# Optimization experiments

Measured on AMD Instinct MI355X. Metric: run time of the kernel, lower is better.

The kernel has to match this reference:

```python
import jax, jax.numpy as jnp
import numpy as np


def spatial_coords(h, w):
    # Vectorized generate_spatial_batch -> [8, h, w]
    ws = jnp.arange(w, dtype=jnp.float32)
    hs = jnp.arange(h, dtype=jnp.float32)
    xmin = ws / w * 2 - 1
    xmax = (ws + 1) / w * 2 - 1
    ymin = hs / h * 2 - 1
    ymax = (hs + 1) / h * 2 - 1
    z = jnp.zeros((h, w), jnp.float32)
    return jnp.stack([
        z + xmin[None, :], z + ymin[:, None], z + xmax[None, :], z + ymax[:, None],
        z + (xmin + xmax)[None, :] / 2, z + (ymin + ymax)[:, None] / 2,
        z + 1.0 / w, z + 1.0 / h], axis=0)


def conv3x3(x, w):
    return jax.lax.conv_general_dilated(x, w, (1, 1), [(1, 1), (1, 1)],
                                        dimension_numbers=('NCHW', 'OIHW', 'NCHW'))


def conv1x1(x, w, b=None):
    y = jnp.einsum('nchw,dc->ndhw', x, w)
    return y if b is None else y + b[None, :, None, None]


def _forward(f_nodes, h_nodes, p_nodes, xp, h_att, p_att,
             dc_q_w, dc_q_b, dc_k_w, dc_k_b, dc_p_w, dc_p_b,
             ctx_w1, ctx_w2, ctx_b2,
             du_a1, du_a2, du_a2b, du_r1, du_r2,
             dl_a1, dl_a2, dl_a2b, dl_r1, dl_r2,
             dp_proj, dp_r1, dp_r2, dp_r2b,
             gru_gw, gru_gb, gru_cw, alpha):
    # BatchNorm (InPlaceABNSync) at default init is identity; relu(leaky_relu(x)) == relu(x).
    N, C, H, W = xp.shape
    coord = spatial_coords(H, W)                      # [8,H,W]
    coord_b = jnp.broadcast_to(coord[None], (N, 8, H, W))
    # Dep_Context: shared key map
    key_f = jax.nn.relu(conv1x1(jnp.concatenate([xp, coord_b], axis=1), dc_k_w, dc_k_b))  # [N,64,H,W]
    xp_flat = xp.reshape(N, C, H * W)
    coord_flat = coord.reshape(8, H * W)
    wq, wk = dc_p_w[:, :64], dc_p_w[:, 64:]           # split project conv over concat channels

    def dep_context(hu_att):                          # hu_att: [N,1,H,W]
        na = jax.nn.softmax(hu_att.reshape(N, H * W), axis=-1)
        hu_c = jnp.einsum('nck,nk->nc', xp_flat, na)  # attention-pooled center [N,C]
        co_c = jnp.einsum('ck,nk->nc', coord_flat, na)
        q = jax.nn.relu(jnp.concatenate([hu_c, co_c], axis=1) @ dc_q_w.T + dc_q_b)  # [N,64]
        energy = (q @ wq.T)[:, :, None, None] + conv1x1(key_f, wk) + dc_p_b[None, :, None, None]
        att = jax.nn.sigmoid(energy)                  # [N,1,H,W]
        inv = 1.0 - hu_att
        return att * inv, att * xp * inv

    dep_att, dep = jax.vmap(dep_context)(p_att[1:])   # [6,N,1,H,W], [6,N,C,H,W]

    # Contexture attention maps (per-part weights); 5 = neighbors per node in full graph
    def ctx_att(da, w1, w2, b2):
        h1 = jax.nn.relu(conv3x3(jnp.concatenate([da, xp], axis=1), w1))
        return conv1x1(h1, w2, b2)                    # [N,5,H,W]

    fdep_att = jax.vmap(ctx_att)(dep_att, ctx_w1, ctx_w2, ctx_b2)  # [6,N,5,H,W]
    att_sm = jax.nn.softmax(fdep_att, axis=2)

    def decomp(parent, children, parent_att, a1, a2, a2b, r1, r2):
        dm = conv1x1(jax.nn.relu(conv3x3(jnp.concatenate([parent_att, xp], axis=1), a1)), a2, a2b)
        da = jax.nn.softmax(dm, axis=1)               # [N,K,H,W]
        def rel(att_i, child):
            x = jnp.concatenate([parent * att_i * parent_att, child], axis=1)
            return jax.nn.relu(conv1x1(jax.nn.relu(conv3x3(x, r1)), r2))
        parts = jax.vmap(rel)(jnp.moveaxis(da, 1, 0)[:, :, None], children)
        return parts, dm

    du_parts, du_att = decomp(h_nodes[1], p_nodes[1:5], h_att[1], du_a1, du_a2, du_a2b, du_r1, du_r2)
    dl_parts, dl_att = decomp(h_nodes[2], p_nodes[5:7], h_att[2], dl_a1, dl_a2, dl_a2b, dl_r1, dl_r2)

    # Dependency messages over the fixed part graph (fully connected, 6 part nodes)
    P = 6
    ea, eb = np.nonzero(1 - np.eye(P, dtype=np.int32))   # row-major == torch.nonzero order
    ce = np.where(eb < ea, eb, eb - 1)                   # index of b in part_list_list[a]
    hv_e = p_nodes[eb]        # NOTE: source indexes p_node_list by raw edge id (no +1) - kept faithful
    hu_e = dep[ea]            # [E,N,C,H,W]
    att_e = att_sm[ea, :, ce][:, :, None]                # [E,N,1,H,W]

    def dep_msg(hv, hu, att):
        m = jax.nn.relu(conv1x1(hu * att, dp_proj))
        y = jax.nn.relu(conv3x3(jnp.concatenate([m, hv], axis=1), dp_r1))
        return jax.nn.sigmoid(conv1x1(y, dp_r2, dp_r2b))

    msgs = jax.vmap(dep_msg)(hv_e, hu_e, att_e)          # [E,N,hid,H,W]
    xpp = jax.ops.segment_sum(msgs, jnp.asarray(eb), num_segments=P)  # [6,N,hid,H,W]

    x_stack = jnp.concatenate([h_nodes[0:1],
                               du_parts + alpha * xpp[0:4],
                               dl_parts + alpha * xpp[4:6]], axis=0)   # [7,N,hid,H,W]

    def gru(x, h, gw, gb, cw):
        g = conv1x1(jnp.concatenate([x, h], axis=1), gw, gb)
        r = jax.nn.sigmoid(g[:, 0:1])
        u = jax.nn.sigmoid(g[:, 1:2])
        cnm = jax.nn.relu(conv1x1(jnp.concatenate([x, r * h], axis=1), cw))
        return (1 - u) * h + u * cnm

    p_new = jax.vmap(gru)(x_stack, p_nodes, gru_gw, gru_gb, gru_cw)
    return (p_new, du_att, dl_att, fdep_att)


def setup_inputs() -> dict:
    key = jax.random.key(0)
    ks = iter(jax.random.split(key, 48))
    def rn(shape, s=0.05):
        return jax.random.normal(next(ks), shape, jnp.float32) * s
    N, C, H, W, HID, P = 2, 256, 48, 48, 10, 7
    return dict(
        f_nodes=rn((2, N, HID, H, W), 1.0),
        h_nodes=rn((3, N, HID, H, W), 1.0),
        p_nodes=rn((P, N, HID, H, W), 1.0),
        xp=rn((N, C, H, W), 1.0),
        h_att=jax.random.uniform(next(ks), (3, N, 1, H, W), jnp.float32),
        p_att=jax.random.uniform(next(ks), (P, N, 1, H, W), jnp.float32),
        dc_q_w=rn((64, C + 8)), dc_q_b=jnp.zeros((64,), jnp.float32),
        dc_k_w=rn((64, C + 8)), dc_k_b=jnp.zeros((64,), jnp.float32),
        dc_p_w=rn((1, 128)), dc_p_b=jnp.zeros((1,), jnp.float32),
        ctx_w1=rn((6, C, C + 1, 3, 3)), ctx_w2=rn((6, 5, C)), ctx_b2=jnp.zeros((6, 5), jnp.float32),
        du_a1=rn((C, C + 1, 3, 3)), du_a2=rn((4, C)), du_a2b=jnp.zeros((4,), jnp.float32),
        du_r1=rn((HID, 2 * HID, 3, 3)), du_r2=rn((HID, HID)),
        dl_a1=rn((C, C + 1, 3, 3)), dl_a2=rn((2, C)), dl_a2b=jnp.zeros((2,), jnp.float32),
        dl_r1=rn((HID, 2 * HID, 3, 3)), dl_r2=rn((HID, HID)),
        dp_proj=rn((HID, C)), dp_r1=rn((HID, 2 * HID, 3, 3)), dp_r2=rn((HID, HID)), dp_r2b=jnp.zeros((HID,), jnp.float32),
        gru_gw=rn((P, 2, 2 * HID)), gru_gb=jnp.zeros((P, 2), jnp.float32), gru_cw=rn((P, HID, 2 * HID)),
        alpha=jnp.ones((1,), jnp.float32),
    )


def reference(f_nodes, h_nodes, p_nodes, xp, h_att, p_att,
              dc_q_w, dc_q_b, dc_k_w, dc_k_b, dc_p_w, dc_p_b,
              ctx_w1, ctx_w2, ctx_b2,
              du_a1, du_a2, du_a2b, du_r1, du_r2,
              dl_a1, dl_a2, dl_a2b, dl_r1, dl_r2,
              dp_proj, dp_r1, dp_r2, dp_r2b,
              gru_gw, gru_gb, gru_cw, alpha):
    return _forward(f_nodes, h_nodes, p_nodes, xp, h_att, p_att,
                    dc_q_w, dc_q_b, dc_k_w, dc_k_b, dc_p_w, dc_p_b,
                    ctx_w1, ctx_w2, ctx_b2,
                    du_a1, du_a2, du_a2b, du_r1, du_r2,
                    dl_a1, dl_a2, dl_a2b, dl_r1, dl_r2,
                    dp_proj, dp_r1, dp_r2, dp_r2b,
                    gru_gw, gru_gb, gru_cw, alpha)
```

## Files before the change

kernel.cpp:

```cpp
#include <hip/hip_runtime.h>
#include <math.h>

constexpr int NB_ = 2;
constexpr int C_  = 256;
constexpr int HW_ = 2304;

typedef float f32x4 __attribute__((ext_vector_type(4)));
typedef short short8 __attribute__((ext_vector_type(8)));

__device__ __forceinline__ float coordval(int c, int k) {
  int y = k / 48, x = k - y * 48;
  switch (c) {
    case 0: return x * (1.f/24.f) - 1.f;
    case 1: return y * (1.f/24.f) - 1.f;
    case 2: return (x + 1) * (1.f/24.f) - 1.f;
    case 3: return (y + 1) * (1.f/24.f) - 1.f;
    case 4: return (x + 0.5f) * (1.f/24.f) - 1.f;
    case 5: return (y + 0.5f) * (1.f/24.f) - 1.f;
    default: return 1.f/48.f;
  }
}

__device__ __forceinline__ float sigmoidf_(float x) { return 1.f / (1.f + expf(-x)); }
__device__ __forceinline__ unsigned short f2bf(float f) {
  unsigned int u = __float_as_uint(f);
  unsigned int r = (u + 0x7FFFu + ((u >> 16) & 1u)) >> 16;
  return (unsigned short)r;
}
__device__ __forceinline__ float bf2f(unsigned short h) {
  return __uint_as_float(((unsigned int)h) << 16);
}

__device__ __forceinline__ void xbf_impl(int bid, char* smem,
    const float* __restrict__ xp, unsigned short* __restrict__ xbf)
{
  float (*xt)[65] = (float(*)[65])smem;
  int t = threadIdx.x;
  int px0 = bid * 64;
  int n = px0 / HW_, k0 = px0 - n * HW_;
  for (int cb = 0; cb < 4; ++cb) {
    __syncthreads();
    for (int i = t; i < 4096; i += 256) {
      int cl = i >> 6, pxl = i & 63;
      xt[cl][pxl] = xp[((size_t)(n * C_ + cb * 64 + cl)) * HW_ + k0 + pxl];
    }
    __syncthreads();
    for (int i = t; i < 4096; i += 256) {
      int pxl = i >> 6, cl = i & 63;
      xbf[((size_t)(n * HW_ + k0 + pxl)) * 256 + cb * 64 + cl] = f2bf(xt[cl][pxl]);
    }
  }
}

__device__ __forceinline__ void wbf_impl(int bid, char* smem,
    const float* __restrict__ ctx_w1, const float* __restrict__ du_a1,
    const float* __restrict__ dl_a1,
    unsigned short* __restrict__ wt, float* __restrict__ w0)
{
  float* sl = (float*)smem;
  int inst = bid >> 8, oc = bid & 255;
  const float* src = (inst < 6) ? (ctx_w1 + (size_t)inst * 256 * 2313)
                   : (inst == 6 ? du_a1 : dl_a1);
  src += (size_t)oc * 2313;
  int t = threadIdx.x;
  for (int i = t; i < 2313; i += 256) sl[i] = src[i];
  __syncthreads();
  int mf = oc >> 4, lr = oc & 15;
  for (int i = t; i < 288; i += 256) {
    int pos = i / 32; int rest = i - pos * 32;
    int chunk = rest >> 2, lg = rest & 3;
    short8 v;
    #pragma unroll
    for (int j = 0; j < 8; ++j) {
      int c = chunk * 32 + lg * 8 + j;
      v[j] = (short)f2bf(sl[(size_t)(c + 1) * 9 + pos]);
    }
    size_t addr = ((((size_t)(inst * 9 + pos) * 8 + chunk) * 16 + mf) << 9)
                  + (size_t)(lg * 16 + lr) * 8;
    *(short8*)(wt + addr) = v;
  }
  if (t < 9) w0[((size_t)inst * 256 + oc) * 9 + t] = sl[t];
}

__device__ __forceinline__ void smhuc_impl(int bid, char* smem,
    const float* __restrict__ xp, const float* __restrict__ p_att,
    float* __restrict__ hu_ws)
{
  float* na  = (float*)smem;
  float* red = (float*)(smem + 9216);
  int cb = bid & 15; int pair = bid >> 4;
  int n = pair % NB_;
  int t = threadIdx.x;
  const float* att = p_att + (size_t)(NB_ + pair) * HW_;

  float m = -1e30f;
  for (int k = t; k < HW_; k += 256) m = fmaxf(m, att[k]);
  #pragma unroll
  for (int off = 32; off > 0; off >>= 1) m = fmaxf(m, __shfl_down(m, off, 64));
  if ((t & 63) == 0) red[t >> 6] = m;
  __syncthreads();
  if (t == 0) { float mm = red[0]; for (int w = 1; w < 4; ++w) mm = fmaxf(mm, red[w]); red[0] = mm; }
  __syncthreads();
  m = red[0];
  float s = 0.f;
  for (int k = t; k < HW_; k += 256) s += expf(att[k] - m);
  #pragma unroll
  for (int off = 32; off > 0; off >>= 1) s += __shfl_down(s, off, 64);
  if ((t & 63) == 0) red[8 + (t >> 6)] = s;
  __syncthreads();
  if (t == 0) { float ss = 0; for (int w = 0; w < 4; ++w) ss += red[8 + w]; red[8] = ss; }
  __syncthreads();
  float inv = 1.f / red[8];
  for (int k = t; k < HW_; k += 256) na[k] = expf(att[k] - m) * inv;
  __syncthreads();

  int wv = t >> 6, l = t & 63;
  #pragma unroll
  for (int cq = 0; cq < 4; ++cq) {
    int c = cb * 16 + wv * 4 + cq;
    const float* x = xp + (size_t)(n * C_ + c) * HW_;
    float a = 0.f;
    for (int k = l; k < HW_; k += 64) a = fmaf(x[k], na[k], a);
    #pragma unroll
    for (int off = 32; off > 0; off >>= 1) a += __shfl_down(a, off, 64);
    if (l == 0) hu_ws[(size_t)pair * 256 + c] = a;
  }
}

__device__ __forceinline__ void yhv_impl(int bid, char* smem,
    const float* __restrict__ p_nodes, const float* __restrict__ dp_r1,
    float* __restrict__ yhv_ws)
{
  float (*xt)[18][20] = (float(*)[18][20])smem;
  float* wl = (float*)(smem + 14400);
  int tile = bid % 9; bid /= 9;
  int n = bid % NB_;  int v = bid / NB_;
  int ty0 = (tile / 3) * 16, tx0 = (tile % 3) * 16;
  int t = threadIdx.x;
  for (int i = t; i < 900; i += 256) {
    int d = i / 90; int rest = i - d * 90; int ic = rest / 9; int pos = rest - ic * 9;
    wl[i] = dp_r1[(d * 20 + 10 + ic) * 9 + pos];
  }
  for (int i = t; i < 10 * 324; i += 256) {
    int d = i / 324; int rr = (i % 324) / 18; int cc = i % 18;
    int gy = ty0 + rr - 1, gx = tx0 + cc - 1;
    float val = 0.f;
    if (gy >= 0 && gy < 48 && gx >= 0 && gx < 48)
      val = p_nodes[((size_t)(v * NB_ + n) * 10 + d) * HW_ + gy * 48 + gx];
    xt[d][rr][cc] = val;
  }
  __syncthreads();
  int rr = t >> 4, cc = t & 15;
  int k = (ty0 + rr) * 48 + tx0 + cc;
  float y[10];
  #pragma unroll
  for (int d = 0; d < 10; ++d) y[d] = 0.f;
  for (int ic = 0; ic < 10; ++ic)
    #pragma unroll
    for (int kh = 0; kh < 3; ++kh)
      #pragma unroll
      for (int kw = 0; kw < 3; ++kw) {
        float xv = xt[ic][rr + kh][cc + kw];
        #pragma unroll
        for (int d = 0; d < 10; ++d)
          y[d] = fmaf(wl[(d * 10 + ic) * 9 + kh * 3 + kw], xv, y[d]);
      }
  #pragma unroll
  for (int d = 0; d < 10; ++d)
    yhv_ws[((size_t)(v * NB_ + n) * 10 + d) * HW_ + k] = y[d];
}

__global__ __launch_bounds__(256) void k_fa(
    const float* __restrict__ xp, unsigned short* __restrict__ xbf,
    const float* __restrict__ ctx_w1, const float* __restrict__ du_a1,
    const float* __restrict__ dl_a1,
    unsigned short* __restrict__ wt, float* __restrict__ w0,
    const float* __restrict__ p_att, float* __restrict__ hu_ws,
    const float* __restrict__ p_nodes, const float* __restrict__ dp_r1,
    float* __restrict__ yhv_ws)
{
  __shared__ __align__(16) char smem[18432];
  int bid = blockIdx.x;
  if (bid < 72)        xbf_impl(bid, smem, xp, xbf);
  else if (bid < 2120) wbf_impl(bid - 72, smem, ctx_w1, du_a1, dl_a1, wt, w0);
  else if (bid < 2312) smhuc_impl(bid - 2120, smem, xp, p_att, hu_ws);
  else                 yhv_impl(bid - 2312, smem, p_nodes, dp_r1, yhv_ws);
}

__device__ __forceinline__ void qdot_impl(int pair, char* smem,
    const float* __restrict__ p_att, const float* __restrict__ hu_ws,
    const float* __restrict__ dc_q_w, const float* __restrict__ dc_q_b,
    const float* __restrict__ dc_p_w, float* __restrict__ qdot)
{
  float* na  = (float*)smem;
  float* red = (float*)(smem + 9216);
  float* co  = (float*)(smem + 9280);
  float* hu  = (float*)(smem + 9312);
  float* ql  = (float*)(smem + 10336);
  int t = threadIdx.x;
  const float* att = p_att + (size_t)(NB_ + pair) * HW_;

  float m = -1e30f;
  for (int k = t; k < HW_; k += 256) m = fmaxf(m, att[k]);
  #pragma unroll
  for (int off = 32; off > 0; off >>= 1) m = fmaxf(m, __shfl_down(m, off, 64));
  if ((t & 63) == 0) red[t >> 6] = m;
  __syncthreads();
  if (t == 0) { float mm = red[0]; for (int w = 1; w < 4; ++w) mm = fmaxf(mm, red[w]); red[0] = mm; }
  __syncthreads();
  m = red[0];
  float s = 0.f;
  for (int k = t; k < HW_; k += 256) s += expf(att[k] - m);
  #pragma unroll
  for (int off = 32; off > 0; off >>= 1) s += __shfl_down(s, off, 64);
  if ((t & 63) == 0) red[8 + (t >> 6)] = s;
  __syncthreads();
  if (t == 0) { float ss = 0; for (int w = 0; w < 4; ++w) ss += red[8 + w]; red[8] = ss; }
  __syncthreads();
  float inv = 1.f / red[8];
  for (int k = t; k < HW_; k += 256) na[k] = expf(att[k] - m) * inv;
  hu[t] = hu_ws[(size_t)pair * 256 + t];
  __syncthreads();

  int wv = t >> 6, l = t & 63;
  #pragma unroll
  for (int q = 0; q < 2; ++q) {
    int cc = wv * 2 + q;
    float a = 0.f;
    for (int k = l; k < HW_; k += 64) a = fmaf(coordval(cc, k), na[k], a);
    #pragma unroll
    for (int off = 32; off > 0; off >>= 1) a += __shfl_down(a, off, 64);
    if (l == 0) co[cc] = a;
  }
  __syncthreads();
  if (t < 64) {
    float a = dc_q_b[t];
    const float* wr = dc_q_w + (size_t)t * 264;
    for (int c = 0; c < 256; ++c) a = fmaf(wr[c], hu[c], a);
    #pragma unroll
    for (int c = 0; c < 8; ++c) a = fmaf(wr[256 + c], co[c], a);
    ql[t] = fmaxf(a, 0.f) * dc_p_w[t];
  }
  __syncthreads();
  if (t == 0) {
    float a = 0.f;
    for (int d = 0; d < 64; ++d) a += ql[d];
    qdot[pair] = a;
  }
}

__device__ __forceinline__ void rpx_impl(int bid, char* smem,
    const unsigned short* __restrict__ xbf, const float* __restrict__ dp_proj,
    float* __restrict__ rpx)
{
  float* pj   = (float*)smem;
  float* part = (float*)(smem + 10240);
  int t = threadIdx.x;
  for (int i = t; i < 2560; i += 256) {
    int d = i >> 8, c = i & 255;
    pj[c * 10 + d] = dp_proj[i];
  }
  __syncthreads();
  int lane = t & 63, q = t >> 6;
  int px = bid * 64 + lane;
  const unsigned short* xr = xbf + (size_t)px * 256;
  float acc[10];
  #pragma unroll
  for (int d = 0; d < 10; ++d) acc[d] = 0.f;
  for (int c8 = q * 8; c8 < q * 8 + 8; ++c8) {
    short8 v = *(const short8*)(xr + c8 * 8);
    #pragma unroll
    for (int j = 0; j < 8; ++j) {
      float f = bf2f((unsigned short)v[j]);
      const float* pc = &pj[(c8 * 8 + j) * 10];
      #pragma unroll
      for (int d = 0; d < 10; ++d) acc[d] = fmaf(pc[d], f, acc[d]);
    }
  }
  if (q) {
    #pragma unroll
    for (int d = 0; d < 10; ++d) part[((q - 1) * 64 + lane) * 10 + d] = acc[d];
  }
  __syncthreads();
  if (t < 64) {
    int p2 = bid * 64 + t;
    int n = p2 / HW_, k = p2 - n * HW_;
    #pragma unroll
    for (int d = 0; d < 10; ++d) {
      float s = acc[d] + part[t * 10 + d] + part[(64 + t) * 10 + d] + part[(128 + t) * 10 + d];
      rpx[((size_t)(n * 10 + d)) * HW_ + k] = fmaxf(s, 0.f);
    }
  }
}

__global__ __launch_bounds__(256) void k_fb(
    const float* __restrict__ p_att, const float* __restrict__ hu_ws,
    const float* __restrict__ dc_q_w, const float* __restrict__ dc_q_b,
    const float* __restrict__ dc_p_w, float* __restrict__ qdot,
    const unsigned short* __restrict__ xbf, const float* __restrict__ dp_proj,
    float* __restrict__ rpx)
{
  __shared__ __align__(16) char smem[18432];
  int bid = blockIdx.x;
  if (bid < 12) qdot_impl(bid, smem, p_att, hu_ws, dc_q_w, dc_q_b, dc_p_w, qdot);
  else          rpx_impl(bid - 12, smem, xbf, dp_proj, rpx);
}

__global__ __launch_bounds__(256) void k_keymma(
    const unsigned short* __restrict__ xbf, const float* __restrict__ dc_k_w,
    const float* __restrict__ dc_k_b, const float* __restrict__ dc_p_w,
    const float* __restrict__ qdot, const float* __restrict__ dc_p_b,
    const float* __restrict__ p_att, float* __restrict__ dep_att)
{
  __shared__ unsigned short wlf[64 * 296];
  __shared__ unsigned short xl[64 * 40];
  int t = threadIdx.x;
  for (int i = t; i < 64 * 264; i += 256) {
    int d = i / 264, c = i - d * 264;
    wlf[d * 296 + c] = f2bf(dc_k_w[i]);
  }
  for (int i = t; i < 64 * 32; i += 256) {
    int d = i >> 5, c = 264 + (i & 31);
    wlf[d * 296 + c] = 0;
  }
  int px0 = blockIdx.x * 64;
  int w = t >> 6, l = t & 63;
  int lr = l & 15, lg = l >> 4;

  f32x4 acc[4];
  #pragma unroll
  for (int mi = 0; mi < 4; ++mi) acc[mi] = (f32x4){0.f,0.f,0.f,0.f};

  for (int ch = 0; ch < 9; ++ch) {
    __syncthreads();
    {
      int i = t;
      int pxl = i >> 2, q = i & 3;
      int px = px0 + pxl, n = px / HW_, k = px - n * HW_;
      int c0 = ch * 32 + q * 8;
      short8 v;
      if (c0 + 7 < 256) {
        v = *(const short8*)(xbf + ((size_t)(n * HW_ + k)) * 256 + c0);
      } else {
        #pragma unroll
        for (int j = 0; j < 8; ++j) {
          int cc = c0 + j;
          float f = (cc < 256) ? bf2f(xbf[((size_t)(n * HW_ + k)) * 256 + cc])
                   : (cc < 264 ? coordval(cc - 256, k) : 0.f);
          v[j] = (short)f2bf(f);
        }
      }
      *(short8*)(xl + pxl * 40 + q * 8) = v;
    }
    __syncthreads();
    short8 bfr = *(const short8*)(xl + (w * 16 + lr) * 40 + lg * 8);
    #pragma unroll
    for (int mi = 0; mi < 4; ++mi) {
      short8 a = *(const short8*)(wlf + (mi * 16 + lr) * 296 + ch * 32 + lg * 8);
      acc[mi] = __builtin_amdgcn_mfma_f32_16x16x32_bf16(a, bfr, acc[mi], 0, 0, 0);
    }
  }

  float s = 0.f;
  #pragma unroll
  for (int mi = 0; mi < 4; ++mi)
    #pragma unroll
    for (int r = 0; r < 4; ++r) {
      int d = mi * 16 + lg * 4 + r;
      s += dc_p_w[64 + d] * fmaxf(acc[mi][r] + dc_k_b[d], 0.f);
    }
  s += __shfl_down(s, 32, 64);
  s += __shfl_down(s, 16, 64);
  if (lg == 0) {
    int px = px0 + w * 16 + lr;
    int n = px / HW_, k = px - n * HW_;
    float base = s + dc_p_b[0];
    #pragma unroll
    for (int e = 0; e < 6; ++e) {
      float energy = qdot[e * NB_ + n] + base;
      float a = sigmoidf_(energy);
      float hu = p_att[(size_t)((1 + e) * NB_ + n) * HW_ + k];
      dep_att[((size_t)(e * NB_ + n)) * HW_ + k] = a * (1.f - hu);
    }
  }
}

__global__ __launch_bounds__(512, 4) void k_convfused(
    const unsigned short* __restrict__ xbf, const unsigned short* __restrict__ wt,
    const float* __restrict__ w0, const float* __restrict__ dep_att,
    const float* __restrict__ h_att,
    const float* __restrict__ ctx_w2, const float* __restrict__ du_a2,
    const float* __restrict__ dl_a2,
    const float* __restrict__ ctx_b2, const float* __restrict__ du_a2b,
    const float* __restrict__ dl_a2b,
    float* __restrict__ out_fdep, float* __restrict__ out_du, float* __restrict__ out_dl,
    float* __restrict__ att_sm, float* __restrict__ da_u, float* __restrict__ da_l)
{
  int bid = blockIdx.x;
  int inst = bid & 7;
  int n = (bid >> 3) & 1;
  int tile = bid >> 4;
  int ty0 = (tile >> 3) * 8;
  int tx0 = (tile & 7) * 6;

  __shared__ __align__(16) unsigned short xs[80 * 256];
  __shared__ float asf[80];

  const float* asrc = (inst < 6) ? dep_att + (size_t)(inst * NB_ + n) * HW_
                    : h_att + (size_t)(((inst == 6) ? 1 : 2) * NB_ + n) * HW_;
  int nd = (inst < 6) ? 5 : (inst == 6 ? 4 : 2);
  const float* w2 = (inst < 6) ? ctx_w2 + (size_t)inst * 5 * 256
                               : (inst == 6 ? du_a2 : dl_a2);

  int t = threadIdx.x;
  const unsigned short* xg = xbf + (size_t)n * HW_ * 256;

  for (int i = t; i < 2560; i += 512) {
    int row = i >> 5, q = i & 31;
    int yy = row >> 3, xx = row & 7;
    int gy = ty0 + yy - 1, gx = tx0 + xx - 1;
    short8 v = (short8){0,0,0,0,0,0,0,0};
    if (gy >= 0 && gy < 48 && gx >= 0 && gx < 48)
      v = *(const short8*)(xg + ((size_t)(gy * 48 + gx)) * 256 + q * 8);
    int s = q ^ (row & 7);
    *(short8*)(xs + row * 256 + s * 8) = v;
  }
  for (int i = t; i < 80; i += 512) {
    int yy = i >> 3, xx = i & 7;
    int gy = ty0 + yy - 1, gx = tx0 + xx - 1;
    asf[i] = (gy >= 0 && gy < 48 && gx >= 0 && gx < 48) ? asrc[gy * 48 + gx] : 0.f;
  }
  __syncthreads();

  int wm = t >> 6;
  int l = t & 63;
  int lr = l & 15, lg = l >> 4;

  f32x4 acc[2][3];
  #pragma unroll
  for (int mi = 0; mi < 2; ++mi)
    #pragma unroll
    for (int nf = 0; nf < 3; ++nf) acc[mi][nf] = (f32x4){0.f,0.f,0.f,0.f};

  int rb[3];
  #pragma unroll
  for (int nf = 0; nf < 3; ++nf) {
    int p = nf * 16 + lr;
    int y = p / 6, x = p - y * 6;
    rb[nf] = y * 8 + x;
  }

  const unsigned short* wta = wt + (((size_t)inst * 72 * 16) << 9)
                              + (((size_t)(wm * 2)) << 9) + (size_t)l * 8;
  short8 av[2], nv[2];
  av[0] = *(const short8*)(wta);
  av[1] = *(const short8*)(wta + 512);

  for (int ch = 0; ch < 8; ++ch) {
    #pragma unroll
    for (int pos = 0; pos < 9; ++pos) {
      {
        int npos = (pos == 8) ? 0 : pos + 1;
        int nch = (pos == 8) ? ((ch + 1 > 7) ? 7 : ch + 1) : ch;
        size_t ofs = ((size_t)((npos * 8 + nch) * 16)) << 9;
        nv[0] = *(const short8*)(wta + ofs);
        nv[1] = *(const short8*)(wta + ofs + 512);
      }
      int koff = (pos / 3) * 8 + (pos % 3);
      short8 bfr[3];
      #pragma unroll
      for (int nf = 0; nf < 3; ++nf) {
        int rowIdx = rb[nf] + koff;
        int s = (ch * 4 + lg) ^ (rowIdx & 7);
        bfr[nf] = *(const short8*)(xs + rowIdx * 256 + s * 8);
      }
      #pragma unroll
      for (int mi = 0; mi < 2; ++mi)
        #pragma unroll
        for (int nf = 0; nf < 3; ++nf)
          acc[mi][nf] = __builtin_amdgcn_mfma_f32_16x16x32_bf16(av[mi], bfr[nf], acc[mi][nf], 0, 0, 0);
      av[0] = nv[0]; av[1] = nv[1];
    }
  }

  __syncthreads();
  float* ovl = (float*)xs;
  float* w0l = ovl;
  float* w2l = ovl + 2304;
  float* sred = ovl + 3584;
  for (int i = t; i < 2304; i += 512) w0l[i] = w0[(size_t)inst * 2304 + i];
  for (int i = t; i < 1280; i += 512) w2l[i] = (i < nd * 256) ? w2[i] : 0.f;
  __syncthreads();

  float pd[3][5];
  #pragma unroll
  for (int nf = 0; nf < 3; ++nf)
    #pragma unroll
    for (int d = 0; d < 5; ++d) pd[nf][d] = 0.f;

  #pragma unroll
  for (int nf = 0; nf < 3; ++nf) {
    #pragma unroll
    for (int mi = 0; mi < 2; ++mi) {
      #pragma unroll
      for (int r = 0; r < 4; ++r) {
        int oc = wm * 32 + mi * 16 + lg * 4 + r;
        float v = acc[mi][nf][r];
        const float* wr = &w0l[oc * 9];
        #pragma unroll
        for (int pos = 0; pos < 9; ++pos) {
          int koff = (pos / 3) * 8 + (pos % 3);
          v = fmaf(wr[pos], asf[rb[nf] + koff], v);
        }
        v = fmaxf(v, 0.f);
        #pragma unroll
        for (int d = 0; d < 5; ++d) pd[nf][d] = fmaf(w2l[d * 256 + oc], v, pd[nf][d]);
      }
    }
  }
  #pragma unroll
  for (int nf = 0; nf < 3; ++nf)
    #pragma unroll
    for (int d = 0; d < 5; ++d) {
      float s = pd[nf][d];
      s += __shfl_down(s, 32, 64);
      s += __shfl_down(s, 16, 64);
      pd[nf][d] = s;
    }
  if (lg == 0) {
    #pragma unroll
    for (int nf = 0; nf < 3; ++nf) {
      int pxi = nf * 16 + lr;
      #pragma unroll
      for (int d = 0; d < 5; ++d)
        sred[(wm * 48 + pxi) * 5 + d] = pd[nf][d];
    }
  }
  __syncthreads();
  if (t < 48) {
    int y = t / 6, x = t - y * 6;
    int gk = (ty0 + y) * 48 + tx0 + x;
    float vals[5];
    float mx = -1e30f;
    for (int d = 0; d < nd; ++d) {
      float s = 0.f;
      #pragma unroll
      for (int wq = 0; wq < 8; ++wq) s += sred[(wq * 48 + t) * 5 + d];
      s += (inst < 6) ? ctx_b2[inst * 5 + d] : (inst == 6 ? du_a2b[d] : dl_a2b[d]);
      vals[d] = s;
      mx = fmaxf(mx, s);
      if (inst < 6)       out_fdep[((size_t)(inst * NB_ + n) * 5 + d) * HW_ + gk] = s;
      else if (inst == 6) out_du[((size_t)n * 4 + d) * HW_ + gk] = s;
      else                out_dl[((size_t)n * 2 + d) * HW_ + gk] = s;
    }
    float ssum = 0.f;
    for (int d = 0; d < nd; ++d) { vals[d] = expf(vals[d] - mx); ssum += vals[d]; }
    float is = 1.f / ssum;
    for (int d = 0; d < nd; ++d) {
      float sm = vals[d] * is;
      if (inst < 6)       att_sm[((size_t)(inst * NB_ + n) * 5 + d) * HW_ + gk] = sm;
      else if (inst == 6) da_u[((size_t)n * 4 + d) * HW_ + gk] = sm;
      else                da_l[((size_t)n * 2 + d) * HW_ + gk] = sm;
    }
  }
}

__global__ __launch_bounds__(256) void k_msgs_edge(
    const float* __restrict__ att_sm, const float* __restrict__ dep_att,
    const float* __restrict__ rpx, const float* __restrict__ yhv_ws,
    const float* __restrict__ dp_r1, const float* __restrict__ dp_r2,
    const float* __restrict__ dp_r2b, float* __restrict__ msg_ws)
{
  int b = blockIdx.x;
  int tile = b % 9; b /= 9;
  int n = b % NB_;  b /= NB_;
  int ui = b % 5;   int v = b / 5;
  int u = (ui < v) ? ui : ui + 1;
  int ce = (v < u) ? v : v - 1;
  int ty0 = (tile / 3) * 16, tx0 = (tile % 3) * 16;

  __shared__ float xt[10][18][20];
  __shared__ float wl[900];
  __shared__ float w2l[100];
  __shared__ float b2l[10];
  int t = threadIdx.x;
  for (int i = t; i < 900; i += 256) {
    int d = i / 90; int rest = i - d * 90; int ic = rest / 9; int pos = rest - ic * 9;
    wl[i] = dp_r1[(d * 20 + ic) * 9 + pos];
  }
  for (int i = t; i < 100; i += 256) w2l[i] = dp_r2[i];
  if (t < 10) b2l[t] = dp_r2b[t];

  const float* asrc = att_sm + ((size_t)(u * NB_ + n) * 5 + ce) * HW_;
  const float* dsrc = dep_att + (size_t)(u * NB_ + n) * HW_;
  for (int i = t; i < 10 * 324; i += 256) {
    int d = i / 324; int rr = (i % 324) / 18; int cc = i % 18;
    int gy = ty0 + rr - 1, gx = tx0 + cc - 1;
    float val = 0.f;
    if (gy >= 0 && gy < 48 && gx >= 0 && gx < 48) {
      int kk = gy * 48 + gx;
      val = asrc[kk] * dsrc[kk] * rpx[((size_t)n * 10 + d) * HW_ + kk];
    }
    xt[d][rr][cc] = val;
  }
  __syncthreads();
  int rr = t >> 4, cc = t & 15;
  int k = (ty0 + rr) * 48 + tx0 + cc;
  float y[10];
  #pragma unroll
  for (int d = 0; d < 10; ++d) y[d] = 0.f;
  for (int ic = 0; ic < 10; ++ic)
    #pragma unroll
    for (int kh = 0; kh < 3; ++kh)
      #pragma unroll
      for (int kw = 0; kw < 3; ++kw) {
        float xv = xt[ic][rr + kh][cc + kw];
        #pragma unroll
        for (int d = 0; d < 10; ++d)
          y[d] = fmaf(wl[(d * 10 + ic) * 9 + kh * 3 + kw], xv, y[d]);
      }
  float s[10];
  #pragma unroll
  for (int d = 0; d < 10; ++d)
    s[d] = fmaxf(y[d] + yhv_ws[((size_t)(v * NB_ + n) * 10 + d) * HW_ + k], 0.f);
  #pragma unroll
  for (int d = 0; d < 10; ++d) {
    float m = b2l[d];
    #pragma unroll
    for (int j = 0; j < 10; ++j) m = fmaf(w2l[d * 10 + j], s[j], m);
    msg_ws[(((size_t)(v * 5 + ui) * NB_ + n) * 10 + d) * HW_ + k] = sigmoidf_(m);
  }
}

__global__ __launch_bounds__(256) void k_parts_gru(
    const float* __restrict__ h_nodes, const float* __restrict__ p_nodes,
    const float* __restrict__ h_att,
    const float* __restrict__ da_u, const float* __restrict__ da_l,
    const float* __restrict__ du_r1, const float* __restrict__ du_r2,
    const float* __restrict__ dl_r1, const float* __restrict__ dl_r2,
    const float* __restrict__ msg_ws, const float* __restrict__ alpha,
    const float* __restrict__ gru_gw, const float* __restrict__ gru_gb,
    const float* __restrict__ gru_cw, float* __restrict__ p_new)
{
  int b = blockIdx.x;
  int tile = b % 9; b /= 9;
  int n = b % NB_;  int vp = b / NB_;
  int ty0 = (tile / 3) * 16, tx0 = (tile % 3) * 16;
  int t = threadIdx.x;
  int rr = t >> 4, cc = t & 15;
  int k = (ty0 + rr) * 48 + tx0 + cc;

  float x[10], h[10];

  if (vp == 0) {
    #pragma unroll
    for (int d = 0; d < 10; ++d) {
      x[d] = h_nodes[((size_t)n * 10 + d) * HW_ + k];
      h[d] = p_nodes[((size_t)n * 10 + d) * HW_ + k];
    }
  } else {
    bool isU = (vp <= 4);
    int j = isU ? vp - 1 : vp - 5;
    const float* parent = h_nodes + ((size_t)((isU ? 1 : 2) * NB_ + n) * 10) * HW_;
    const float* patt   = h_att + (size_t)((isU ? 1 : 2) * NB_ + n) * HW_;
    const float* da     = isU ? (da_u + ((size_t)n * 4 + j) * HW_) : (da_l + ((size_t)n * 2 + j) * HW_);
    const float* child  = p_nodes + (size_t)(vp * NB_ + n) * 10 * HW_;
    const float* r1 = isU ? du_r1 : dl_r1;
    const float* r2 = isU ? du_r2 : dl_r2;

    __shared__ float xt[20][18][20];
    __shared__ float wl[1800];
    __shared__ float w2l[100];
    for (int i = t; i < 1800; i += 256) wl[i] = r1[i];
    for (int i = t; i < 100; i += 256) w2l[i] = r2[i];
    for (int i = t; i < 20 * 324; i += 256) {
      int d = i / 324; int r2i = (i % 324) / 18; int c2 = i % 18;
      int gy = ty0 + r2i - 1, gx = tx0 + c2 - 1;
      float val = 0.f;
      if (gy >= 0 && gy < 48 && gx >= 0 && gx < 48) {
        int kk = gy * 48 + gx;
        val = (d < 10) ? parent[(size_t)d * HW_ + kk] * da[kk] * patt[kk]
                       : child[(size_t)(d - 10) * HW_ + kk];
      }
      xt[d][r2i][c2] = val;
    }
    __syncthreads();
    float y[10];
    #pragma unroll
    for (int d = 0; d < 10; ++d) y[d] = 0.f;
    for (int ic = 0; ic < 20; ++ic)
      #pragma unroll
      for (int kh = 0; kh < 3; ++kh)
        #pragma unroll
        for (int kw = 0; kw < 3; ++kw) {
          float xv = xt[ic][rr + kh][cc + kw];
          #pragma unroll
          for (int d = 0; d < 10; ++d)
            y[d] = fmaf(wl[(d * 20 + ic) * 9 + kh * 3 + kw], xv, y[d]);
        }
    float yr[10];
    #pragma unroll
    for (int d = 0; d < 10; ++d) yr[d] = fmaxf(y[d], 0.f);

    float al = alpha[0];
    int v = vp - 1;
    #pragma unroll
    for (int d = 0; d < 10; ++d) {
      float s = 0.f;
      #pragma unroll
      for (int jj = 0; jj < 10; ++jj) s = fmaf(w2l[d * 10 + jj], yr[jj], s);
      float parts = fmaxf(s, 0.f);
      float xs = 0.f;
      #pragma unroll
      for (int ui = 0; ui < 5; ++ui)
        xs += msg_ws[(((size_t)(v * 5 + ui) * NB_ + n) * 10 + d) * HW_ + k];
      x[d] = parts + al * xs;
      h[d] = p_nodes[((size_t)(vp * NB_ + n) * 10 + d) * HW_ + k];
    }
  }

  const float* gw = gru_gw + (size_t)vp * 40;
  const float* gb = gru_gb + (size_t)vp * 2;
  const float* cw = gru_cw + (size_t)vp * 200;
  float g0 = gb[0], g1 = gb[1];
  #pragma unroll
  for (int d = 0; d < 10; ++d) {
    g0 = fmaf(gw[d], x[d], fmaf(gw[10 + d], h[d], g0));
    g1 = fmaf(gw[20 + d], x[d], fmaf(gw[30 + d], h[d], g1));
  }
  float rg = sigmoidf_(g0);
  float ug = sigmoidf_(g1);
  #pragma unroll
  for (int d = 0; d < 10; ++d) {
    float s = 0.f;
    const float* cr = cw + d * 20;
    #pragma unroll
    for (int jj = 0; jj < 10; ++jj)
      s = fmaf(cr[jj], x[jj], fmaf(cr[10 + jj], rg * h[jj], s));
    float cn = fmaxf(s, 0.f);
    p_new[((size_t)(vp * NB_ + n) * 10 + d) * HW_ + k] = (1.f - ug) * h[d] + ug * cn;
  }
}

extern "C" void kernel_launch(void* const* d_in, const int* in_sizes, int n_in,
                              void* d_out, int out_size, void* d_ws, size_t ws_size,
                              hipStream_t stream) {
  (void)in_sizes; (void)n_in; (void)out_size; (void)ws_size;
  const float* h_nodes = (const float*)d_in[1];
  const float* p_nodes = (const float*)d_in[2];
  const float* xp      = (const float*)d_in[3];
  const float* h_att   = (const float*)d_in[4];
  const float* p_att   = (const float*)d_in[5];
  const float* dc_q_w  = (const float*)d_in[6];
  const float* dc_q_b  = (const float*)d_in[7];
  const float* dc_k_w  = (const float*)d_in[8];
  const float* dc_k_b  = (const float*)d_in[9];
  const float* dc_p_w  = (const float*)d_in[10];
  const float* dc_p_b  = (const float*)d_in[11];
  const float* ctx_w1  = (const float*)d_in[12];
  const float* ctx_w2  = (const float*)d_in[13];
  const float* ctx_b2  = (const float*)d_in[14];
  const float* du_a1   = (const float*)d_in[15];
  const float* du_a2   = (const float*)d_in[16];
  const float* du_a2b  = (const float*)d_in[17];
  const float* du_r1   = (const float*)d_in[18];
  const float* du_r2   = (const float*)d_in[19];
  const float* dl_a1   = (const float*)d_in[20];
  const float* dl_a2   = (const float*)d_in[21];
  const float* dl_a2b  = (const float*)d_in[22];
  const float* dl_r1   = (const float*)d_in[23];
  const float* dl_r2   = (const float*)d_in[24];
  const float* dp_proj = (const float*)d_in[25];
  const float* dp_r1   = (const float*)d_in[26];
  const float* dp_r2   = (const float*)d_in[27];
  const float* dp_r2b  = (const float*)d_in[28];
  const float* gru_gw  = (const float*)d_in[29];
  const float* gru_gb  = (const float*)d_in[30];
  const float* gru_cw  = (const float*)d_in[31];
  const float* alpha   = (const float*)d_in[32];

  float* ws = (float*)d_ws;
  float* qdot    = ws + 4608;
  float* dep_att = ws + 4624;
  float* rpx     = ws + 32272;
  float* att_sm  = ws + 78352;
  float* da_u    = ws + 216592;
  float* da_l    = ws + 235024;
  float* yhv_ws  = ws + 244240;
  float* w0      = ws + 520720;
  float* hu_ws   = att_sm + 27648;
  unsigned short* us = (unsigned short*)(ws + 539152);
  unsigned short* xbf = us;
  unsigned short* wt  = us + 1179648;
  float* msg_ws = (float*)(us + 5898240);

  float* out      = (float*)d_out;
  float* out_pnew = out;
  float* out_du   = out + 322560;
  float* out_dl   = out + 340992;
  float* out_fdep = out + 350208;

  k_fa<<<2420, 256, 0, stream>>>(xp, xbf, ctx_w1, du_a1, dl_a1, wt, w0,
                                 p_att, hu_ws, p_nodes, dp_r1, yhv_ws);
  k_fb<<<84, 256, 0, stream>>>(p_att, hu_ws, dc_q_w, dc_q_b, dc_p_w, qdot,
                               xbf, dp_proj, rpx);
  k_keymma<<<72, 256, 0, stream>>>(xbf, dc_k_w, dc_k_b, dc_p_w,
                                   qdot, dc_p_b, p_att, dep_att);
  k_convfused<<<768, 512, 0, stream>>>(xbf, wt, w0, dep_att, h_att,
                                       ctx_w2, du_a2, dl_a2, ctx_b2, du_a2b, dl_a2b,
                                       out_fdep, out_du, out_dl, att_sm, da_u, da_l);
  k_msgs_edge<<<540, 256, 0, stream>>>(att_sm, dep_att, rpx, yhv_ws,
                                       dp_r1, dp_r2, dp_r2b, msg_ws);
  k_parts_gru<<<126, 256, 0, stream>>>(h_nodes, p_nodes, h_att, da_u, da_l,
                                       du_r1, du_r2, dl_r1, dl_r2, msg_ws, alpha,
                                       gru_gw, gru_gb, gru_cw, out_pnew);
}
```

Before: 212.7 us.

## Reshape conv tile to 6x8 and precompute attention products in shared memory

The fused 3x3 conv kernel now uses 6-row by 8-column pixel tiles instead of 8x6, so the halo is 8x10. Each tile row then spans 8 contiguous pixels, which gives more contiguous global loads and output stores. The message kernels first compute the per-pixel attention product (att*dep or da*patt) once into a small shared buffer and reuse it across all channels. This removes repeated global loads at the cost of one extra barrier. The halo still holds exactly 80 rows, so the shared memory layout and the XOR swizzle are unchanged.

Result: faster. 200.3 us (-5.8%).

```diff
diff --git a/kernel.cpp b/kernel.cpp
--- a/kernel.cpp
+++ b/kernel.cpp
@@ -400,8 +400,8 @@
   int inst = bid & 7;
   int n = (bid >> 3) & 1;
   int tile = bid >> 4;
-  int ty0 = (tile >> 3) * 8;
-  int tx0 = (tile & 7) * 6;
+  int ty0 = (tile / 6) * 6;
+  int tx0 = (tile % 6) * 8;
 
   __shared__ __align__(16) unsigned short xs[80 * 256];
   __shared__ float asf[80];
@@ -417,7 +417,7 @@
 
   for (int i = t; i < 2560; i += 512) {
     int row = i >> 5, q = i & 31;
-    int yy = row >> 3, xx = row & 7;
+    int yy = row / 10, xx = row - yy * 10;
     int gy = ty0 + yy - 1, gx = tx0 + xx - 1;
     short8 v = (short8){0,0,0,0,0,0,0,0};
     if (gy >= 0 && gy < 48 && gx >= 0 && gx < 48)
@@ -426,7 +426,7 @@
     *(short8*)(xs + row * 256 + s * 8) = v;
   }
   for (int i = t; i < 80; i += 512) {
-    int yy = i >> 3, xx = i & 7;
+    int yy = i / 10, xx = i - yy * 10;
     int gy = ty0 + yy - 1, gx = tx0 + xx - 1;
     asf[i] = (gy >= 0 && gy < 48 && gx >= 0 && gx < 48) ? asrc[gy * 48 + gx] : 0.f;
   }
@@ -446,8 +446,8 @@
   #pragma unroll
   for (int nf = 0; nf < 3; ++nf) {
     int p = nf * 16 + lr;
-    int y = p / 6, x = p - y * 6;
-    rb[nf] = y * 8 + x;
+    int y = p >> 3, x = p & 7;
+    rb[nf] = y * 10 + x;
   }
 
   const unsigned short* wta = wt + (((size_t)inst * 72 * 16) << 9)
@@ -466,7 +466,7 @@
         nv[0] = *(const short8*)(wta + ofs);
         nv[1] = *(const short8*)(wta + ofs + 512);
       }
-      int koff = (pos / 3) * 8 + (pos % 3);
+      int koff = (pos / 3) * 10 + (pos % 3);
       short8 bfr[3];
       #pragma unroll
       for (int nf = 0; nf < 3; ++nf) {
@@ -509,7 +509,7 @@
         const float* wr = &w0l[oc * 9];
         #pragma unroll
         for (int pos = 0; pos < 9; ++pos) {
-          int koff = (pos / 3) * 8 + (pos % 3);
+          int koff = (pos / 3) * 10 + (pos % 3);
           v = fmaf(wr[pos], asf[rb[nf] + koff], v);
         }
         v = fmaxf(v, 0.f);
@@ -538,7 +538,7 @@
   }
   __syncthreads();
   if (t < 48) {
-    int y = t / 6, x = t - y * 6;
+    int y = t >> 3, x = t & 7;
     int gk = (ty0 + y) * 48 + tx0 + x;
     float vals[5];
     float mx = -1e30f;
@@ -580,6 +580,7 @@
   int ty0 = (tile / 3) * 16, tx0 = (tile % 3) * 16;
 
   __shared__ float xt[10][18][20];
+  __shared__ float ad[324];
   __shared__ float wl[900];
   __shared__ float w2l[100];
   __shared__ float b2l[10];
@@ -593,13 +594,24 @@
 
   const float* asrc = att_sm + ((size_t)(u * NB_ + n) * 5 + ce) * HW_;
   const float* dsrc = dep_att + (size_t)(u * NB_ + n) * HW_;
-  for (int i = t; i < 10 * 324; i += 256) {
-    int d = i / 324; int rr = (i % 324) / 18; int cc = i % 18;
+  for (int i = t; i < 324; i += 256) {
+    int rr = i / 18, cc = i - (i / 18) * 18;
     int gy = ty0 + rr - 1, gx = tx0 + cc - 1;
     float val = 0.f;
     if (gy >= 0 && gy < 48 && gx >= 0 && gx < 48) {
       int kk = gy * 48 + gx;
-      val = asrc[kk] * dsrc[kk] * rpx[((size_t)n * 10 + d) * HW_ + kk];
+      val = asrc[kk] * dsrc[kk];
+    }
+    ad[i] = val;
+  }
+  __syncthreads();
+  for (int i = t; i < 10 * 324; i += 256) {
+    int d = i / 324; int r = i - d * 324; int rr = r / 18; int cc = r - rr * 18;
+    int gy = ty0 + rr - 1, gx = tx0 + cc - 1;
+    float val = 0.f;
+    if (gy >= 0 && gy < 48 && gx >= 0 && gx < 48) {
+      int kk = gy * 48 + gx;
+      val = ad[r] * rpx[((size_t)n * 10 + d) * HW_ + kk];
     }
     xt[d][rr][cc] = val;
   }
@@ -669,17 +681,29 @@
     const float* r2 = isU ? du_r2 : dl_r2;
 
     __shared__ float xt[20][18][20];
+    __shared__ float dpl[324];
     __shared__ float wl[1800];
     __shared__ float w2l[100];
     for (int i = t; i < 1800; i += 256) wl[i] = r1[i];
     for (int i = t; i < 100; i += 256) w2l[i] = r2[i];
-    for (int i = t; i < 20 * 324; i += 256) {
-      int d = i / 324; int r2i = (i % 324) / 18; int c2 = i % 18;
+    for (int i = t; i < 324; i += 256) {
+      int r2i = i / 18, c2 = i - (i / 18) * 18;
       int gy = ty0 + r2i - 1, gx = tx0 + c2 - 1;
       float val = 0.f;
       if (gy >= 0 && gy < 48 && gx >= 0 && gx < 48) {
         int kk = gy * 48 + gx;
-        val = (d < 10) ? parent[(size_t)d * HW_ + kk] * da[kk] * patt[kk]
+        val = da[kk] * patt[kk];
+      }
+      dpl[i] = val;
+    }
+    __syncthreads();
+    for (int i = t; i < 20 * 324; i += 256) {
+      int d = i / 324; int r = i - d * 324; int r2i = r / 18; int c2 = r - r2i * 18;
+      int gy = ty0 + r2i - 1, gx = tx0 + c2 - 1;
+      float val = 0.f;
+      if (gy >= 0 && gy < 48 && gx >= 0 && gx < 48) {
+        int kk = gy * 48 + gx;
+        val = (d < 10) ? parent[(size_t)d * HW_ + kk] * dpl[r]
                        : child[(size_t)(d - 10) * HW_ + kk];
       }
       xt[d][r2i][c2] = val;
```
